# Optimization experiments

Hardware: AMD Instinct MI355X
Metric: run time of the kernel (lower is better)

Reference implementation:

```python
import math
import jax, jax.numpy as jnp
import numpy as np

B, S, D = 4, 2048, 1024
N_HEAD = 16


def setup_inputs() -> dict:
    key = jax.random.key(0)
    k1, k2 = jax.random.split(key)
    x = jax.random.normal(k1, (B, S, D), dtype=jnp.float32)
    # xavier-uniform style scale for the fused QKV kernel
    limit = math.sqrt(6.0 / (D + 3 * D))
    W_qkv = jax.random.uniform(k2, (D, 3 * D), dtype=jnp.float32, minval=-limit, maxval=limit)
    b_qkv = jnp.zeros((3 * D,), dtype=jnp.float32)
    return {"x": x, "W_qkv": W_qkv, "b_qkv": b_qkv}


def reference(x, W_qkv, b_qkv):
    batch_size, seq_len, d_model = x.shape
    head_dim = d_model // N_HEAD
    # fused QKV projection: [B, S, 3D]
    qkv = jnp.einsum('bsd,de->bse', x, W_qkv) + b_qkv
    qkv = qkv.reshape(batch_size, seq_len, N_HEAD, 3 * head_dim)
    qkv = qkv.transpose(0, 2, 1, 3)  # [B, H, S, 3*hd]
    q, k, v = jnp.split(qkv, 3, axis=-1)
    # scaled dot-product attention with causal mask
    attn_logits = jnp.einsum('bhqd,bhkd->bhqk', q, k) / math.sqrt(head_dim)
    causal = jnp.tril(jnp.ones((seq_len, seq_len), dtype=jnp.float32))[None, None]
    attn_logits = jnp.where(causal == 0, -jnp.inf, attn_logits)
    attn = jax.nn.softmax(attn_logits, axis=-1)
    out = jnp.einsum('bhqk,bhkd->bhqd', attn, v)  # [B, H, S, hd]
    out = out.transpose(0, 2, 1, 3).reshape(batch_size, seq_len, -1)
    return out
```

## Files before the change

### kernel.cpp

```cpp
#include <hip/hip_runtime.h>
#include <hip/hip_bf16.h>
#include <cstdint>

typedef __bf16 bf16x8 __attribute__((ext_vector_type(8)));
typedef float f32x4 __attribute__((ext_vector_type(4)));
typedef float f32x16 __attribute__((ext_vector_type(16)));

__device__ inline unsigned short f2bf(float f) {
    union { float f; unsigned int u; } v; v.f = f;
    unsigned int u = v.u;
    unsigned int r = (u + 0x7FFFu + ((u >> 16) & 1u)) >> 16;
    return (unsigned short)r;
}

__device__ inline f32x4 mfma16(bf16x8 a, bf16x8 b, f32x4 c) {
    return __builtin_amdgcn_mfma_f32_16x16x32_bf16(a, b, c, 0, 0, 0);
}

__device__ inline f32x16 mfma32(bf16x8 a, bf16x8 b, f32x16 c) {
    return __builtin_amdgcn_mfma_f32_32x32x16_bf16(a, b, c, 0, 0, 0);
}

__device__ inline bf16x8 ldfrag(const unsigned short* p) {
    uint4 v = *(const uint4*)p;
    return __builtin_bit_cast(bf16x8, v);
}

__device__ inline void cp16(const unsigned short* g, unsigned short* l) {
    __builtin_amdgcn_global_load_lds(
        (const __attribute__((address_space(1))) unsigned int*)g,
        (__attribute__((address_space(3))) unsigned int*)l,
        16, 0, 0);
}

__device__ inline unsigned int pkbf(float a, float b) {
    return __builtin_amdgcn_perm(__builtin_bit_cast(unsigned int, b),
                                 __builtin_bit_cast(unsigned int, a),
                                 0x07060302u);
}

__device__ inline void plswap(unsigned int& a, unsigned int& b) {
    typedef unsigned int u32x2 __attribute__((ext_vector_type(2)));
    u32x2 r = __builtin_amdgcn_permlane32_swap(a, b, false, false);
    a = r[0]; b = r[1];
}

__global__ void k_convert_x(const float* __restrict__ in,
                            unsigned short* __restrict__ out, int n4) {
    int i = blockIdx.x * blockDim.x + threadIdx.x;
    if (i < n4) {
        float4 f = ((const float4*)in)[i];
        ushort4 o;
        o.x = f2bf(f.x); o.y = f2bf(f.y); o.z = f2bf(f.z); o.w = f2bf(f.w);
        ((ushort4*)out)[i] = o;
    }
}

__global__ void k_transpose_w(const float* __restrict__ W,
                              unsigned short* __restrict__ Wt) {
    __shared__ float tile[32][33];
    int nt = blockIdx.x, kt = blockIdx.y;
    int tx = threadIdx.x & 31, ty = threadIdx.x >> 5;
#pragma unroll
    for (int yy = 0; yy < 4; ++yy) {
        int y = ty + yy * 8;
        tile[y][tx] = W[(size_t)(kt * 32 + y) * 3072 + nt * 32 + tx];
    }
    __syncthreads();
#pragma unroll
    for (int yy = 0; yy < 4; ++yy) {
        int nrow = ty + yy * 8;
        Wt[(size_t)(nt * 32 + nrow) * 1024 + kt * 32 + tx] = f2bf(tile[tx][nrow]);
    }
}

__global__ __launch_bounds__(512, 2) void k_qkv_gemm(
    const unsigned short* __restrict__ A,
    const unsigned short* __restrict__ Bt,
    const float* __restrict__ bias,
    unsigned short* __restrict__ C) {
    __shared__ __align__(16) unsigned short As[3 * 256 * 64];
    __shared__ __align__(16) unsigned short Bs[3 * 128 * 64];
    const int tid = threadIdx.x;
    const int lane = tid & 63;
    const int w = tid >> 6;
    const int wm = w >> 1, wn = w & 1;
    const int l31 = lane & 31;
    const int hi = lane >> 5;
    const int xr7 = l31 & 7;
    const int m0 = blockIdx.y * 256;
    const int n0 = blockIdx.x * 128;

    const int srow = tid >> 3, sseg = tid & 7;
    const int gsw = (sseg ^ (srow & 7)) * 8;
    const unsigned short* pA = A + (size_t)(m0 + srow) * 1024 + gsw;
    const unsigned short* pB = Bt + (size_t)(n0 + srow) * 1024 + gsw;

    f32x16 acc[2][2] = {};

    auto stage = [&](int buf, int k0) {
        unsigned short* da = &As[buf * 16384 + tid * 8];
        unsigned short* db = &Bs[buf * 8192 + tid * 8];
#pragma unroll
        for (int i = 0; i < 4; ++i)
            cp16(pA + (size_t)i * 64 * 1024 + k0, da + i * 4096);
#pragma unroll
        for (int j = 0; j < 2; ++j)
            cp16(pB + (size_t)j * 64 * 1024 + k0, db + j * 4096);
    };

    stage(0, 0);
    stage(1, 64);

    for (int kt = 0; kt < 16; ++kt) {
        const int buf = kt % 3;
        if (kt == 15)
            asm volatile("s_waitcnt vmcnt(0)" ::: "memory");
        else
            asm volatile("s_waitcnt vmcnt(6)" ::: "memory");
        __builtin_amdgcn_s_barrier();
        if (kt + 2 < 16) stage((kt + 2) % 3, (kt + 2) * 64);

        const unsigned short* ab = &As[buf * 16384];
        const unsigned short* bb = &Bs[buf * 8192];
        bf16x8 af[2][4], bfr[2][4];
#pragma unroll
        for (int rb = 0; rb < 2; ++rb) {
            const int r = wm * 64 + rb * 32 + l31;
#pragma unroll
            for (int ks = 0; ks < 4; ++ks)
                af[rb][ks] = ldfrag(ab + r * 64 + ((ks * 2 + hi) ^ xr7) * 8);
        }
#pragma unroll
        for (int cb = 0; cb < 2; ++cb) {
            const int r = wn * 64 + cb * 32 + l31;
#pragma unroll
            for (int ks = 0; ks < 4; ++ks)
                bfr[cb][ks] = ldfrag(bb + r * 64 + ((ks * 2 + hi) ^ xr7) * 8);
        }
#pragma unroll
        for (int rb = 0; rb < 2; ++rb)
#pragma unroll
            for (int cb = 0; cb < 2; ++cb)
#pragma unroll
                for (int ks = 0; ks < 4; ++ks)
                    acc[rb][cb] = mfma32(af[rb][ks], bfr[cb][ks], acc[rb][cb]);

        asm volatile("s_waitcnt lgkmcnt(0)" ::: "memory");
    }

#pragma unroll
    for (int cb = 0; cb < 2; ++cb) {
        const int col = n0 + wn * 64 + cb * 32 + l31;
        const float bv = bias[col];
#pragma unroll
        for (int rb = 0; rb < 2; ++rb) {
            const int rbase = m0 + wm * 64 + rb * 32 + 4 * hi;
#pragma unroll
            for (int g = 0; g < 4; ++g)
#pragma unroll
                for (int rr = 0; rr < 4; ++rr) {
                    const int row = rbase + g * 8 + rr;
                    C[(size_t)row * 3072 + col] =
                        f2bf(acc[rb][cb][g * 4 + rr] + bv);
                }
        }
    }
}

__global__ __launch_bounds__(256) void k_transpose_v(
    const unsigned short* __restrict__ qkv,
    unsigned short* __restrict__ VtG) {
    __shared__ unsigned short t[64][65];
    const int st = blockIdx.x;
    const int h = blockIdx.y;
    const int b = blockIdx.z;
    const int tid = threadIdx.x;
    const int voff = h * 192 + 128;
    const size_t base = (size_t)b * 2048 * 3072;
#pragma unroll
    for (int i = 0; i < 2; ++i) {
        int c = tid + i * 256;
        int row = c >> 3, seg = c & 7;
        uint4 v = *(const uint4*)(qkv + base + (size_t)(st * 64 + row) * 3072 + voff + seg * 8);
        unsigned short u8[8];
        *(uint4*)u8 = v;
#pragma unroll
        for (int u = 0; u < 8; ++u) t[row][seg * 8 + u] = u8[u];
    }
    __syncthreads();
    const size_t obase = ((size_t)(b * 16 + h) * 64) * 2048 + st * 64;
#pragma unroll
    for (int i = 0; i < 2; ++i) {
        int c = tid + i * 256;
        int drow = c >> 3, seg = c & 7;
        unsigned short u8[8];
#pragma unroll
        for (int u = 0; u < 8; ++u) u8[u] = t[seg * 8 + u][drow];
        *(uint4*)(VtG + obase + (size_t)drow * 2048 + seg * 8) = *(uint4*)u8;
    }
}

__global__ __launch_bounds__(256) void k_attn(
    const unsigned short* __restrict__ qkv,
    const unsigned short* __restrict__ VtG,
    float* __restrict__ out) {
    const int p = blockIdx.x;
    const int hb = p & 63;
    const int h = hb & 15;
    const int b = hb >> 4;
    const int qt = 31 - (p >> 6);
    const int tid = threadIdx.x;
    const int lane = tid & 63;
    const int w = tid >> 6;
    const int wm = w >> 1;
    const int wn = w & 1;
    const int l31 = lane & 31;
    const int hi = lane >> 5;

    __shared__ __align__(16) unsigned short KsF[2 * 64 * 64];
    __shared__ __align__(16) unsigned short VsF[2 * 64 * 64];

    const size_t base = (size_t)b * 2048 * 3072;
    const int qoff = h * 192, koff = h * 192 + 64;
    const size_t vtbase = (size_t)(b * 16 + h) * 64 * 2048;

    const int srow0 = tid >> 3, sseg = tid & 7;
    const int gsw = (sseg ^ (srow0 & 7)) * 8;
    unsigned short* kd0 = &KsF[tid * 8];
    unsigned short* kd1 = &KsF[2048 + tid * 8];
    unsigned short* vd0 = &VsF[tid * 8];
    unsigned short* vd1 = &VsF[2048 + tid * 8];

    const int xr7 = l31 & 7;
    const int kfbase = (32 * wm + l31) * 64;
    const int vfb0 = l31 * 64;
    const int vfb1 = (32 + l31) * 64;
    const int qcol = 32 * wn + l31;

    const float sc = 0.125f * 1.44269504088896340736f;

    const int qrow = qt * 64 + qcol;
    const unsigned short* qp = qkv + base + (size_t)qrow * 3072 + qoff + hi * 8;
    bf16x8 bq[4];
#pragma unroll
    for (int t = 0; t < 4; ++t) bq[t] = ldfrag(qp + t * 16);

    const unsigned short* kp0 = qkv + base + koff + (size_t)srow0 * 3072 + gsw;
    const unsigned short* kp1 = kp0 + (size_t)32 * 3072;
    const unsigned short* vp0 = VtG + vtbase + (size_t)srow0 * 2048 + gsw;
    const unsigned short* vp1 = vp0 + (size_t)32 * 2048;

    f32x16 acc0 = {0,0,0,0,0,0,0,0,0,0,0,0,0,0,0,0};
    f32x16 acc1 = {0,0,0,0,0,0,0,0,0,0,0,0,0,0,0,0};
    float ptot = 0.f;

    cp16(kp0, kd0); cp16(kp1, kd1); cp16(vp0, vd0); cp16(vp1, vd1);
    __syncthreads();

    for (int kt = 0; kt <= qt; ++kt) {
        const int bo = (kt & 1) * 4096;
        const int bn = bo ^ 4096;
        if (kt < qt) {
            kp0 += 64 * 3072; kp1 += 64 * 3072;
            vp0 += 64;        vp1 += 64;
            cp16(kp0, kd0 + bn); cp16(kp1, kd1 + bn);
            cp16(vp0, vd0 + bn); cp16(vp1, vd1 + bn);
        }

        f32x16 s = {0,0,0,0,0,0,0,0,0,0,0,0,0,0,0,0};
#pragma unroll
        for (int t = 0; t < 4; ++t) {
            const unsigned short* ka =
                &KsF[bo + kfbase + ((2 * t + hi) ^ xr7) * 8];
            s = mfma32(ldfrag(ka), bq[t], s);
        }

        if (kt == qt) {
#pragma unroll
            for (int r = 0; r < 16; ++r) {
                const int srow = 32 * wm + (r & 3) + 8 * (r >> 2) + 4 * hi;
                if (srow > qcol) s[r] = -3.0e38f;
            }
        }

        float pvv[16];
#pragma unroll
        for (int r = 0; r < 16; ++r) {
            pvv[r] = __builtin_amdgcn_exp2f(
                __builtin_fmaf(s[r], sc, -16.0f));
            ptot += pvv[r];
        }
        unsigned int pk0 = pkbf(pvv[0], pvv[1]),   pk1 = pkbf(pvv[2], pvv[3]);
        unsigned int pk2 = pkbf(pvv[4], pvv[5]),   pk3 = pkbf(pvv[6], pvv[7]);
        unsigned int pk4 = pkbf(pvv[8], pvv[9]),   pk5 = pkbf(pvv[10], pvv[11]);
        unsigned int pk6 = pkbf(pvv[12], pvv[13]), pk7 = pkbf(pvv[14], pvv[15]);
        plswap(pk0, pk2); plswap(pk1, pk3);
        plswap(pk4, pk6); plswap(pk5, pk7);
        uint4 w0; w0.x = pk0; w0.y = pk1; w0.z = pk2; w0.w = pk3;
        uint4 w1; w1.x = pk4; w1.y = pk5; w1.z = pk6; w1.w = pk7;
        const bf16x8 pf0 = __builtin_bit_cast(bf16x8, w0);
        const bf16x8 pf1 = __builtin_bit_cast(bf16x8, w1);

        const int su0 = ((4 * wm + hi) ^ xr7) * 8;
        const int su1 = ((4 * wm + 2 + hi) ^ xr7) * 8;
        acc0 = mfma32(ldfrag(&VsF[bo + vfb0 + su0]), pf0, acc0);
        acc0 = mfma32(ldfrag(&VsF[bo + vfb0 + su1]), pf1, acc0);
        acc1 = mfma32(ldfrag(&VsF[bo + vfb1 + su0]), pf0, acc1);
        acc1 = mfma32(ldfrag(&VsF[bo + vfb1 + su1]), pf1, acc1);

        __syncthreads();
    }

    float* Sc = (float*)KsF;
    float* Pt = (float*)VsF;
    const int lb = (wn * 64 + lane) * 8;
    if (wm == 1) {
#pragma unroll
        for (int g = 0; g < 4; ++g) {
            float4 v;
            v.x = acc0[g * 4 + 0]; v.y = acc0[g * 4 + 1];
            v.z = acc0[g * 4 + 2]; v.w = acc0[g * 4 + 3];
            ((float4*)Sc)[lb + (g ^ (lane & 7))] = v;
        }
#pragma unroll
        for (int g = 0; g < 4; ++g) {
            float4 v;
            v.x = acc1[g * 4 + 0]; v.y = acc1[g * 4 + 1];
            v.z = acc1[g * 4 + 2]; v.w = acc1[g * 4 + 3];
            ((float4*)Sc)[lb + ((g + 4) ^ (lane & 7))] = v;
        }
        Pt[wn * 64 + lane] = ptot;
    }
    __syncthreads();
    if (wm == 0) {
#pragma unroll
        for (int g = 0; g < 4; ++g) {
            float4 v = ((const float4*)Sc)[lb + (g ^ (lane & 7))];
            acc0[g * 4 + 0] += v.x; acc0[g * 4 + 1] += v.y;
            acc0[g * 4 + 2] += v.z; acc0[g * 4 + 3] += v.w;
        }
#pragma unroll
        for (int g = 0; g < 4; ++g) {
            float4 v = ((const float4*)Sc)[lb + ((g + 4) ^ (lane & 7))];
            acc1[g * 4 + 0] += v.x; acc1[g * 4 + 1] += v.y;
            acc1[g * 4 + 2] += v.z; acc1[g * 4 + 3] += v.w;
        }
        float l = ptot + Pt[wn * 64 + lane];
        l += __shfl_xor(l, 32, 64);
        const float inv = __builtin_amdgcn_rcpf(l);
        float* op = out + ((size_t)b * 2048 + qrow) * 1024 + h * 64 + 4 * hi;
#pragma unroll
        for (int g = 0; g < 4; ++g) {
            float4 v;
            v.x = acc0[g * 4 + 0] * inv; v.y = acc0[g * 4 + 1] * inv;
            v.z = acc0[g * 4 + 2] * inv; v.w = acc0[g * 4 + 3] * inv;
            *(float4*)(op + g * 8) = v;
        }
#pragma unroll
        for (int g = 0; g < 4; ++g) {
            float4 v;
            v.x = acc1[g * 4 + 0] * inv; v.y = acc1[g * 4 + 1] * inv;
            v.z = acc1[g * 4 + 2] * inv; v.w = acc1[g * 4 + 3] * inv;
            *(float4*)(op + 32 + g * 8) = v;
        }
    }
}

extern "C" void kernel_launch(void* const* d_in, const int* in_sizes, int n_in,
                              void* d_out, int out_size, void* d_ws, size_t ws_size,
                              hipStream_t stream) {
    const float* x = (const float*)d_in[0];
    const float* W = (const float*)d_in[1];
    const float* bq = (const float*)d_in[2];
    float* out = (float*)d_out;

    unsigned short* xbf = (unsigned short*)d_ws;
    unsigned short* wtbf = xbf + (size_t)8192 * 1024;
    unsigned short* qkvbf = wtbf + (size_t)3072 * 1024;
    unsigned short* VtG = xbf;

    k_convert_x<<<8192, 256, 0, stream>>>(x, xbf, 8192 * 1024 / 4);
    k_transpose_w<<<dim3(96, 32), 256, 0, stream>>>(W, wtbf);
    k_qkv_gemm<<<dim3(24, 32), 512, 0, stream>>>(xbf, wtbf, bq, qkvbf);
    k_transpose_v<<<dim3(32, 16, 4), 256, 0, stream>>>(qkvbf, VtG);
    k_attn<<<2048, 256, 0, stream>>>(qkvbf, VtG, out);
}
```

Baseline: 224.8 us.

## Fuse prep kernels and retile QKV GEMM to 128x192 with double buffering

Merges the x-to-bf16 conversion and the W transpose into one launch, removing a kernel launch. Retiles the QKV GEMM from 256x128 tiles with 512 threads and a 3-stage buffer to 128x192 tiles with 256 threads and a 2-stage buffer. Each warp now computes 2x3 MFMA 32x32 blocks, and the grid grows to 1024 blocks for better CU fill. In exchange it waits for all loads and hits a barrier on every k-step, which shortens prefetch overlap.

```diff
diff --git a/kernel.cpp b/kernel.cpp
--- a/kernel.cpp
+++ b/kernel.cpp
@@ -45,42 +45,42 @@
     a = r[0]; b = r[1];
 }
 
-__global__ void k_convert_x(const float* __restrict__ in,
-                            unsigned short* __restrict__ out, int n4) {
-    int i = blockIdx.x * blockDim.x + threadIdx.x;
-    if (i < n4) {
-        float4 f = ((const float4*)in)[i];
+__global__ __launch_bounds__(256) void k_prep(
+    const float* __restrict__ x, unsigned short* __restrict__ xbf,
+    const float* __restrict__ W, unsigned short* __restrict__ Wt) {
+    __shared__ float tile[32][33];
+    if (blockIdx.x < 8192) {
+        int i = blockIdx.x * 256 + threadIdx.x;
+        float4 f = ((const float4*)x)[i];
         ushort4 o;
         o.x = f2bf(f.x); o.y = f2bf(f.y); o.z = f2bf(f.z); o.w = f2bf(f.w);
-        ((ushort4*)out)[i] = o;
-    }
-}
-
-__global__ void k_transpose_w(const float* __restrict__ W,
-                              unsigned short* __restrict__ Wt) {
-    __shared__ float tile[32][33];
-    int nt = blockIdx.x, kt = blockIdx.y;
-    int tx = threadIdx.x & 31, ty = threadIdx.x >> 5;
-#pragma unroll
-    for (int yy = 0; yy < 4; ++yy) {
-        int y = ty + yy * 8;
-        tile[y][tx] = W[(size_t)(kt * 32 + y) * 3072 + nt * 32 + tx];
-    }
-    __syncthreads();
-#pragma unroll
-    for (int yy = 0; yy < 4; ++yy) {
-        int nrow = ty + yy * 8;
-        Wt[(size_t)(nt * 32 + nrow) * 1024 + kt * 32 + tx] = f2bf(tile[tx][nrow]);
-    }
-}
-
-__global__ __launch_bounds__(512, 2) void k_qkv_gemm(
+        ((ushort4*)xbf)[i] = o;
+    } else {
+        int bid = blockIdx.x - 8192;
+        int nt = bid % 96, kt = bid / 96;
+        int tx = threadIdx.x & 31, ty = threadIdx.x >> 5;
+#pragma unroll
+        for (int yy = 0; yy < 4; ++yy) {
+            int y = ty + yy * 8;
+            tile[y][tx] = W[(size_t)(kt * 32 + y) * 3072 + nt * 32 + tx];
+        }
+        __syncthreads();
+#pragma unroll
+        for (int yy = 0; yy < 4; ++yy) {
+            int nrow = ty + yy * 8;
+            Wt[(size_t)(nt * 32 + nrow) * 1024 + kt * 32 + tx] =
+                f2bf(tile[tx][nrow]);
+        }
+    }
+}
+
+__global__ __launch_bounds__(256, 2) void k_qkv_gemm(
     const unsigned short* __restrict__ A,
     const unsigned short* __restrict__ Bt,
     const float* __restrict__ bias,
     unsigned short* __restrict__ C) {
-    __shared__ __align__(16) unsigned short As[3 * 256 * 64];
-    __shared__ __align__(16) unsigned short Bs[3 * 128 * 64];
+    __shared__ __align__(16) unsigned short As[2 * 128 * 64];
+    __shared__ __align__(16) unsigned short Bs[2 * 192 * 64];
     const int tid = threadIdx.x;
     const int lane = tid & 63;
     const int w = tid >> 6;
@@ -88,42 +88,38 @@
     const int l31 = lane & 31;
     const int hi = lane >> 5;
     const int xr7 = l31 & 7;
-    const int m0 = blockIdx.y * 256;
-    const int n0 = blockIdx.x * 128;
+    const int m0 = blockIdx.y * 128;
+    const int n0 = blockIdx.x * 192;
 
     const int srow = tid >> 3, sseg = tid & 7;
     const int gsw = (sseg ^ (srow & 7)) * 8;
     const unsigned short* pA = A + (size_t)(m0 + srow) * 1024 + gsw;
     const unsigned short* pB = Bt + (size_t)(n0 + srow) * 1024 + gsw;
 
-    f32x16 acc[2][2] = {};
+    f32x16 acc[2][3] = {};
 
     auto stage = [&](int buf, int k0) {
-        unsigned short* da = &As[buf * 16384 + tid * 8];
-        unsigned short* db = &Bs[buf * 8192 + tid * 8];
+        unsigned short* da = &As[buf * 8192 + tid * 8];
+        unsigned short* db = &Bs[buf * 12288 + tid * 8];
 #pragma unroll
         for (int i = 0; i < 4; ++i)
-            cp16(pA + (size_t)i * 64 * 1024 + k0, da + i * 4096);
-#pragma unroll
-        for (int j = 0; j < 2; ++j)
-            cp16(pB + (size_t)j * 64 * 1024 + k0, db + j * 4096);
+            cp16(pA + (size_t)i * 32 * 1024 + k0, da + i * 2048);
+#pragma unroll
+        for (int j = 0; j < 6; ++j)
+            cp16(pB + (size_t)j * 32 * 1024 + k0, db + j * 2048);
     };
 
     stage(0, 0);
-    stage(1, 64);
+    asm volatile("s_waitcnt vmcnt(0)" ::: "memory");
+    __builtin_amdgcn_s_barrier();
 
     for (int kt = 0; kt < 16; ++kt) {
-        const int buf = kt % 3;
-        if (kt == 15)
-            asm volatile("s_waitcnt vmcnt(0)" ::: "memory");
-        else
-            asm volatile("s_waitcnt vmcnt(6)" ::: "memory");
-        __builtin_amdgcn_s_barrier();
-        if (kt + 2 < 16) stage((kt + 2) % 3, (kt + 2) * 64);
-
-        const unsigned short* ab = &As[buf * 16384];
-        const unsigned short* bb = &Bs[buf * 8192];
-        bf16x8 af[2][4], bfr[2][4];
+        const int buf = kt & 1;
+        if (kt < 15) stage(buf ^ 1, (kt + 1) * 64);
+
+        const unsigned short* ab = &As[buf * 8192];
+        const unsigned short* bb = &Bs[buf * 12288];
+        bf16x8 af[2][4], bfr[3][4];
 #pragma unroll
         for (int rb = 0; rb < 2; ++rb) {
             const int r = wm * 64 + rb * 32 + l31;
@@ -132,8 +128,8 @@
                 af[rb][ks] = ldfrag(ab + r * 64 + ((ks * 2 + hi) ^ xr7) * 8);
         }
 #pragma unroll
-        for (int cb = 0; cb < 2; ++cb) {
-            const int r = wn * 64 + cb * 32 + l31;
+        for (int cb = 0; cb < 3; ++cb) {
+            const int r = wn * 96 + cb * 32 + l31;
 #pragma unroll
             for (int ks = 0; ks < 4; ++ks)
                 bfr[cb][ks] = ldfrag(bb + r * 64 + ((ks * 2 + hi) ^ xr7) * 8);
@@ -141,17 +137,18 @@
 #pragma unroll
         for (int rb = 0; rb < 2; ++rb)
 #pragma unroll
-            for (int cb = 0; cb < 2; ++cb)
+            for (int cb = 0; cb < 3; ++cb)
 #pragma unroll
                 for (int ks = 0; ks < 4; ++ks)
                     acc[rb][cb] = mfma32(af[rb][ks], bfr[cb][ks], acc[rb][cb]);
 
-        asm volatile("s_waitcnt lgkmcnt(0)" ::: "memory");
-    }
-
-#pragma unroll
-    for (int cb = 0; cb < 2; ++cb) {
-        const int col = n0 + wn * 64 + cb * 32 + l31;
+        asm volatile("s_waitcnt vmcnt(0)" ::: "memory");
+        __builtin_amdgcn_s_barrier();
+    }
+
+#pragma unroll
+    for (int cb = 0; cb < 3; ++cb) {
+        const int col = n0 + wn * 96 + cb * 32 + l31;
         const float bv = bias[col];
 #pragma unroll
         for (int rb = 0; rb < 2; ++rb) {
@@ -380,9 +377,8 @@
     unsigned short* qkvbf = wtbf + (size_t)3072 * 1024;
     unsigned short* VtG = xbf;
 
-    k_convert_x<<<8192, 256, 0, stream>>>(x, xbf, 8192 * 1024 / 4);
-    k_transpose_w<<<dim3(96, 32), 256, 0, stream>>>(W, wtbf);
-    k_qkv_gemm<<<dim3(24, 32), 512, 0, stream>>>(xbf, wtbf, bq, qkvbf);
+    k_prep<<<8192 + 3072, 256, 0, stream>>>(x, xbf, W, wtbf);
+    k_qkv_gemm<<<dim3(16, 64), 256, 0, stream>>>(xbf, wtbf, bq, qkvbf);
     k_transpose_v<<<dim3(32, 16, 4), 256, 0, stream>>>(qkvbf, VtG);
     k_attn<<<2048, 256, 0, stream>>>(qkvbf, VtG, out);
 }
```

Result: faster. 218.9 us (-2.6%).
